# Optimization experiments

Measured on AMD Instinct MI355X. Metric: run time of the kernel, lower is better.

Reference implementation:

```python
import jax, jax.numpy as jnp
import numpy as np

HDIM = 128
SCALE = HDIM ** (-0.5)


def setup_inputs() -> dict:
    key = jax.random.key(0)
    ks = jax.random.split(key, 6)
    B, H, I, J, D = 4, 16, 2048, 2048, HDIM
    q = jax.random.normal(ks[0], (B, H, I, D), dtype=jnp.float32)
    kv = jax.random.normal(ks[1], (B, H, J, D), dtype=jnp.float32)
    # torch nn.Linear weights stored as [out_features, in_features]
    Wq = jax.random.normal(ks[2], (D, D), dtype=jnp.float32) * (D ** -0.5)
    Wkv = jax.random.normal(ks[3], (2 * D, D), dtype=jnp.float32) * (D ** -0.5)
    Wout = jax.random.normal(ks[4], (D, D), dtype=jnp.float32) * (D ** -0.5)
    bout = jax.random.normal(ks[5], (D,), dtype=jnp.float32) * 0.01
    return {"q": q, "kv": kv, "Wq": Wq, "Wkv": Wkv, "Wout": Wout, "bout": bout}


def reference(q, kv, Wq, Wkv, Wout, bout):
    # projections (torch Linear: x @ W.T)
    qp = jnp.einsum('bhid,ed->bhie', q, Wq)
    kvp = jnp.einsum('bhjd,ed->bhje', kv, Wkv)
    k, v = jnp.split(kvp, 2, axis=-1)
    # scaled dot-product cross attention, full score matrix [b,h,i,j]
    dots = jnp.einsum('bhid,bhjd->bhij', qp, k) * SCALE
    attn = jax.nn.softmax(dots, axis=-1)
    out = jnp.einsum('bhij,bhjd->bhid', attn, v)
    # output projection (dropout is identity at inference)
    return jnp.einsum('bhid,ed->bhie', out, Wout) + bout
```

## Files before the change

### kernel.cpp

```cpp
#include <hip/hip_runtime.h>
#include <hip/hip_bf16.h>
#include <math.h>

typedef __attribute__((ext_vector_type(8))) short bf16x8;
typedef __attribute__((ext_vector_type(4))) unsigned short u16x4;
typedef __attribute__((ext_vector_type(4))) float f32x4;

#define MFMA16(a, b, c) __builtin_amdgcn_mfma_f32_16x16x32_bf16(a, b, c, 0, 0, 0)

__device__ inline unsigned short f2bf(float x) {
  union { float f; unsigned u; } v; v.f = x;
  unsigned r = v.u + 0x7FFFu + ((v.u >> 16) & 1u);
  return (unsigned short)(r >> 16);
}

__device__ inline float exp2a(float x) {
  float r;
  asm("v_exp_f32 %0, %1" : "=v"(r) : "v"(x));
  return r;
}

__device__ inline void dma16(const unsigned short* g, unsigned short* l) {
  __builtin_amdgcn_global_load_lds(
      (const __attribute__((address_space(1))) unsigned int*)g,
      (__attribute__((address_space(3))) unsigned int*)l, 16, 0, 0);
}

__device__ unsigned short g_wbf[49152];

__global__ __launch_bounds__(256) void conv_w(
    const float* __restrict__ Wq, const float* __restrict__ Wkv)
{
  int idx = (blockIdx.x * 256 + threadIdx.x) * 4;
  const float* src; int off;
  if (idx < 16384) { src = Wq;  off = idx; }
  else             { src = Wkv; off = idx - 16384; }
  float4 v = *(const float4*)(src + off);
  u16x4 pk;
  pk.x = f2bf(v.x); pk.y = f2bf(v.y); pk.z = f2bf(v.z); pk.w = f2bf(v.w);
  *(u16x4*)&g_wbf[idx] = pk;
}

__global__ __launch_bounds__(256) void proj_q(
    const float* __restrict__ A, unsigned short* __restrict__ out0, float scale)
{
  const int mbase = blockIdx.x * 64;
  const unsigned short* Wb = g_wbf;

  __shared__ unsigned short a_s[64 * 136];
  __shared__ unsigned short w_s[128 * 136];

  const int tid = threadIdx.x;
  for (int p = 0; p < 8; ++p) {
    int r = p * 8 + (tid >> 5);
    int c = tid & 31;
    float4 v = ((const float4*)(A + (size_t)(mbase + r) * 128))[c];
    u16x4 pk;
    pk.x = f2bf(v.x); pk.y = f2bf(v.y); pk.z = f2bf(v.z); pk.w = f2bf(v.w);
    *(u16x4*)&a_s[r * 136 + c * 4] = pk;
  }
  {
    int r0 = tid >> 4, c = (tid & 15) * 8;
    for (int p = 0; p < 8; ++p) {
      int r = p * 16 + r0;
      *(bf16x8*)&w_s[r * 136 + c] = *(const bf16x8*)(Wb + (size_t)r * 128 + c);
    }
  }
  __syncthreads();

  const int wave = tid >> 6, lane = tid & 63, quad = lane >> 4, lr = lane & 15;
  f32x4 zero = {0.f, 0.f, 0.f, 0.f};
  f32x4 acc[8];
  for (int nb = 0; nb < 8; ++nb) acc[nb] = zero;
  for (int ks = 0; ks < 4; ++ks) {
    bf16x8 af = *(const bf16x8*)&a_s[(wave * 16 + lr) * 136 + ks * 32 + quad * 8];
    for (int nb = 0; nb < 8; ++nb) {
      bf16x8 bf = *(const bf16x8*)&w_s[(nb * 16 + lr) * 136 + ks * 32 + quad * 8];
      acc[nb] = MFMA16(af, bf, acc[nb]);
    }
  }
  for (int nb = 0; nb < 8; ++nb)
    for (int r = 0; r < 4; ++r) {
      int row = mbase + wave * 16 + quad * 4 + r;
      int col = nb * 16 + lr;
      out0[(size_t)row * 128 + col] = f2bf(acc[nb][r] * scale);
    }
}

__global__ __launch_bounds__(256) void proj_kv(
    const float* __restrict__ A,
    unsigned short* __restrict__ outK, unsigned short* __restrict__ outVT)
{
  const int mbase = blockIdx.x * 64;
  __shared__ unsigned short a_s[64 * 136];
  __shared__ unsigned short w_s[128 * 136];
  const int tid = threadIdx.x;

  for (int p = 0; p < 8; ++p) {
    int r = p * 8 + (tid >> 5);
    int c = tid & 31;
    float4 v = ((const float4*)(A + (size_t)(mbase + r) * 128))[c];
    u16x4 pk;
    pk.x = f2bf(v.x); pk.y = f2bf(v.y); pk.z = f2bf(v.z); pk.w = f2bf(v.w);
    *(u16x4*)&a_s[r * 136 + c * 4] = pk;
  }

  const int wave = tid >> 6, lane = tid & 63, quad = lane >> 4, lr = lane & 15;
  f32x4 zero = {0.f, 0.f, 0.f, 0.f};

  for (int nt = 0; nt < 2; ++nt) {
    __syncthreads();
    {
      const unsigned short* Wb = g_wbf + 16384 + nt * 16384;
      int r0 = tid >> 4, c = (tid & 15) * 8;
      for (int p = 0; p < 8; ++p) {
        int r = p * 16 + r0;
        *(bf16x8*)&w_s[r * 136 + c] = *(const bf16x8*)(Wb + (size_t)r * 128 + c);
      }
    }
    __syncthreads();

    f32x4 acc[8];
    for (int nb = 0; nb < 8; ++nb) acc[nb] = zero;
    for (int ks = 0; ks < 4; ++ks) {
      bf16x8 af = *(const bf16x8*)&a_s[(wave * 16 + lr) * 136 + ks * 32 + quad * 8];
      for (int nb = 0; nb < 8; ++nb) {
        bf16x8 bf = *(const bf16x8*)&w_s[(nb * 16 + lr) * 136 + ks * 32 + quad * 8];
        acc[nb] = MFMA16(af, bf, acc[nb]);
      }
    }

    if (nt == 0) {
      for (int nb = 0; nb < 8; ++nb)
        for (int r = 0; r < 4; ++r) {
          int row = mbase + wave * 16 + quad * 4 + r;
          int col = nb * 16 + lr;
          outK[(size_t)row * 128 + col] = f2bf(acc[nb][r]);
        }
    } else {
      int gm = mbase + wave * 16 + quad * 4;
      int bh = gm >> 11;
      int j  = gm & 2047;
      unsigned short* vt = outVT + (size_t)bh * 128 * 2048;
      for (int nb = 0; nb < 8; ++nb) {
        int col = nb * 16 + lr;
        u16x4 pk;
        pk.x = f2bf(acc[nb][0]); pk.y = f2bf(acc[nb][1]);
        pk.z = f2bf(acc[nb][2]); pk.w = f2bf(acc[nb][3]);
        *(u16x4*)&vt[(size_t)col * 2048 + j] = pk;
      }
    }
  }
}

__global__ __launch_bounds__(512, 2) void attn_fused(
    const unsigned short* __restrict__ qp,
    const unsigned short* __restrict__ kb,
    const unsigned short* __restrict__ vTb,
    const float* __restrict__ Wout,
    const float* __restrict__ bias,
    float* __restrict__ out)
{
  const int xcd = blockIdx.x & 7;
  const int loc = blockIdx.x >> 3;
  const int qt  = loc & 7;
  const int bh  = (loc >> 3) * 8 + xcd;
  const unsigned short* Q  = qp  + (size_t)bh * 2048 * 128 + (size_t)qt * 256 * 128;
  const unsigned short* K  = kb  + (size_t)bh * 2048 * 128;
  const unsigned short* VT = vTb + (size_t)bh * 128 * 2048;
  float* OUT = out + (size_t)bh * 2048 * 128 + (size_t)qt * 256 * 128;

  __shared__ unsigned short k_s [2][64 * 128];
  __shared__ unsigned short vT_s[2][128 * 64];
  __shared__ unsigned short p_s [256 * 64];
  __shared__ float redu_s[8][2][16];
  __shared__ unsigned short wout_s[128 * 136];

  const int tid = threadIdx.x;
  const int wave = tid >> 6, lane = tid & 63, quad = lane >> 4, lr = lane & 15;

  const int kw_i = wave * 2;
  const int rk0  = 4 * kw_i + (lane >> 4);
  const int rk1  = 4 * (kw_i + 1) + (lane >> 4);
  const int kgo0 = rk0 * 128 + ((lane & 15) ^ (rk0 & 15)) * 8;
  const int kgo1 = rk1 * 128 + ((lane & 15) ^ (rk1 & 15)) * 8;
  const int rv0  = 8 * kw_i + (lane >> 3);
  const int rv1  = 8 * (kw_i + 1) + (lane >> 3);
  const int vsc  = ((lane & 7) ^ ((lane >> 3) & 7)) * 8;
  const int vgo0 = rv0 * 2048 + vsc;
  const int vgo1 = rv1 * 2048 + vsc;
  const int klds0 = kw_i * 512, klds1 = kw_i * 512 + 512;

#define ISSUE_K(T, BUF) do { \
    const unsigned short* _kt = K + (size_t)(T) * 8192; \
    dma16(_kt + kgo0, &k_s[BUF][klds0]); \
    dma16(_kt + kgo1, &k_s[BUF][klds1]); } while (0)
#define ISSUE_V(T, BUF) do { \
    const unsigned short* _vt = VT + (size_t)(T) * 64; \
    dma16(_vt + vgo0, &vT_s[BUF][klds0]); \
    dma16(_vt + vgo1, &vT_s[BUF][klds1]); } while (0)

  bf16x8 qf[2][4];
#pragma unroll
  for (int mb = 0; mb < 2; ++mb)
#pragma unroll
    for (int ks = 0; ks < 4; ++ks)
      qf[mb][ks] = *(const bf16x8*)(Q + (size_t)(wave * 32 + mb * 16 + lr) * 128 + ks * 32 + quad * 8);
  __builtin_amdgcn_sched_barrier(0);
  ISSUE_K(0, 0);
  ISSUE_V(0, 0);
  ISSUE_K(1, 1);
  __builtin_amdgcn_sched_barrier(0);

  f32x4 zero = {0.f, 0.f, 0.f, 0.f};
  f32x4 o_acc[2][8];
  float m_i[2], l_i[2];
#pragma unroll
  for (int mb = 0; mb < 2; ++mb) {
#pragma unroll
    for (int db = 0; db < 8; ++db) o_acc[mb][db] = zero;
    m_i[mb] = -1e30f; l_i[mb] = 0.f;
  }
  int rescM = 0;

  asm volatile("s_waitcnt vmcnt(2)" ::: "memory");
  __builtin_amdgcn_s_barrier();
  __builtin_amdgcn_sched_barrier(0);
  ISSUE_V(1, 1);

#define STEP(JT, BUF) do { \
    f32x4 sT[2][4]; \
    _Pragma("unroll") \
    for (int mi = 0; mi < 2; ++mi) \
      _Pragma("unroll") \
      for (int jb = 0; jb < 4; ++jb) sT[mi][jb] = zero; \
    __builtin_amdgcn_s_setprio(1); \
    _Pragma("unroll") \
    for (int ks = 0; ks < 4; ++ks) { \
      _Pragma("unroll") \
      for (int jb = 0; jb < 4; ++jb) { \
        bf16x8 kfj = *(const bf16x8*)&k_s[BUF][(jb * 16 + lr) * 128 + (((ks * 4 + quad) ^ lr) << 3)]; \
        sT[0][jb] = MFMA16(kfj, qf[0][ks], sT[0][jb]); \
        sT[1][jb] = MFMA16(kfj, qf[1][ks], sT[1][jb]); \
      } \
    } \
    __builtin_amdgcn_s_setprio(0); \
    _Pragma("unroll") \
    for (int mi = 0; mi < 2; ++mi) { \
      const int mb = mi; \
      float mx = fmaxf(fmaxf(sT[mi][0][0], sT[mi][0][1]), fmaxf(sT[mi][0][2], sT[mi][0][3])); \
      _Pragma("unroll") \
      for (int jb = 1; jb < 4; ++jb) \
        mx = fmaxf(mx, fmaxf(fmaxf(sT[mi][jb][0], sT[mi][jb][1]), \
                             fmaxf(sT[mi][jb][2], sT[mi][jb][3]))); \
      mx = fmaxf(mx, __shfl_xor(mx, 16)); \
      mx = fmaxf(mx, __shfl_xor(mx, 32)); \
      if (!__all(mx - m_i[mb] <= 8.f)) {            \
        float mnew = fmaxf(m_i[mb], mx); \
        float alpha = exp2a(m_i[mb] - mnew); \
        m_i[mb] = mnew; \
        l_i[mb] *= alpha; \
        if (lane < 16) redu_s[wave][mb][lane] = alpha; \
        rescM |= (1 << (mb)); \
      } \
      float rs = 0.f; \
      const int prow = wave * 32 + mb * 16 + lr; \
      _Pragma("unroll") \
      for (int jb = 0; jb < 4; ++jb) { \
        float p0 = exp2a(sT[mi][jb][0] - m_i[mb]); \
        float p1 = exp2a(sT[mi][jb][1] - m_i[mb]); \
        float p2 = exp2a(sT[mi][jb][2] - m_i[mb]); \
        float p3 = exp2a(sT[mi][jb][3] - m_i[mb]); \
        rs += (p0 + p1) + (p2 + p3); \
        u16x4 pk; \
        pk.x = f2bf(p0); pk.y = f2bf(p1); pk.z = f2bf(p2); pk.w = f2bf(p3); \
        int c = jb * 2 + (quad >> 1); \
        *(u16x4*)&p_s[prow * 64 + ((c ^ (lr & 7)) << 3) + ((quad & 1) << 2)] = pk; \
      } \
      rs += __shfl_xor(rs, 16); \
      rs += __shfl_xor(rs, 32); \
      l_i[mb] += rs; \
    } \
    __builtin_amdgcn_s_barrier();         \
    __builtin_amdgcn_sched_barrier(0); \
    if ((JT) <= 29) ISSUE_K((JT) + 2, BUF); \
    _Pragma("unroll") \
    for (int mb = 0; mb < 2; ++mb) \
      if (rescM & (1 << (mb))) {                       \
        f32x4 av = *(const f32x4*)&redu_s[wave][mb][quad * 4]; \
        _Pragma("unroll") \
        for (int db = 0; db < 8; ++db) o_acc[mb][db] *= av; \
      } \
    rescM = 0; \
    __builtin_amdgcn_s_setprio(1); \
    _Pragma("unroll") \
    for (int ks2 = 0; ks2 < 2; ++ks2) { \
      const int pc = ((ks2 * 4 + quad) ^ (lr & 7)) << 3; \
      bf16x8 pf[2]; \
      _Pragma("unroll") \
      for (int mb = 0; mb < 2; ++mb) \
        pf[mb] = *(const bf16x8*)&p_s[(wave * 32 + mb * 16 + lr) * 64 + pc]; \
      _Pragma("unroll") \
      for (int db = 0; db < 8; ++db) { \
        bf16x8 vf = *(const bf16x8*)&vT_s[BUF][(db * 16 + lr) * 64 + pc]; \
        _Pragma("unroll") \
        for (int mb = 0; mb < 2; ++mb) \
          o_acc[mb][db] = MFMA16(pf[mb], vf, o_acc[mb][db]); \
      } \
    } \
    __builtin_amdgcn_s_setprio(0); \
    if ((JT) >= 30) { asm volatile("s_waitcnt vmcnt(0)" ::: "memory"); } \
    else            { asm volatile("s_waitcnt vmcnt(2)" ::: "memory"); } \
    __builtin_amdgcn_s_barrier();         \
    __builtin_amdgcn_sched_barrier(0); \
    if ((JT) <= 29) ISSUE_V((JT) + 2, BUF); \
  } while (0)

#pragma unroll 1
  for (int jtb = 0; jtb < 16; ++jtb) {
    const int jt0 = jtb * 2;
    STEP(jt0, 0);
    STEP(jt0 + 1, 1);
  }
#undef STEP
#undef ISSUE_K
#undef ISSUE_V

#pragma unroll
  for (int p = 0; p < 4; ++p) {
    int r = p * 32 + (tid >> 4);
    int c = (tid & 15) * 8;
    float4 v0 = *(const float4*)(Wout + (size_t)r * 128 + c);
    float4 v1 = *(const float4*)(Wout + (size_t)r * 128 + c + 4);
    u16x4 pk0, pk1;
    pk0.x = f2bf(v0.x); pk0.y = f2bf(v0.y); pk0.z = f2bf(v0.z); pk0.w = f2bf(v0.w);
    pk1.x = f2bf(v1.x); pk1.y = f2bf(v1.y); pk1.z = f2bf(v1.z); pk1.w = f2bf(v1.w);
    *(u16x4*)&wout_s[r * 136 + c] = pk0;
    *(u16x4*)&wout_s[r * 136 + c + 4] = pk1;
  }

#pragma unroll
  for (int mb = 0; mb < 2; ++mb)
    if (lane < 16) redu_s[wave][mb][lane] = l_i[mb];
#pragma unroll
  for (int mb = 0; mb < 2; ++mb) {
    f32x4 l4 = *(const f32x4*)&redu_s[wave][mb][quad * 4];
    f32x4 invv;
#pragma unroll
    for (int r = 0; r < 4; ++r) invv[r] = 1.f / l4[r];
#pragma unroll
    for (int db = 0; db < 8; ++db) o_acc[mb][db] *= invv;
  }

  __syncthreads();

  f32x4 acc2[2][8];
#pragma unroll
  for (int mb = 0; mb < 2; ++mb)
#pragma unroll
    for (int nb = 0; nb < 8; ++nb) acc2[mb][nb] = zero;

#pragma unroll
  for (int h = 0; h < 2; ++h) {
#pragma unroll
    for (int mb = 0; mb < 2; ++mb)
#pragma unroll
      for (int db2 = 0; db2 < 4; ++db2) {
        f32x4 o = o_acc[mb][h * 4 + db2];
#pragma unroll
        for (int r = 0; r < 4; ++r) {
          int row = mb * 16 + quad * 4 + r;
          int colh = db2 * 16 + lr;
          int chunk = colh >> 3, off = colh & 7;
          p_s[(wave * 32 + row) * 64 + ((chunk ^ (row & 7)) << 3) + off] = f2bf(o[r]);
        }
      }
#pragma unroll
    for (int ks = 0; ks < 2; ++ks) {
#pragma unroll
      for (int mb = 0; mb < 2; ++mb) {
        int arow = mb * 16 + lr;
        int kk = ks * 32 + quad * 8;
        int chunk = kk >> 3;
        bf16x8 af = *(const bf16x8*)&p_s[(wave * 32 + arow) * 64 + ((chunk ^ (arow & 7)) << 3)];
#pragma unroll
        for (int nb = 0; nb < 8; ++nb) {
          bf16x8 bf = *(const bf16x8*)&wout_s[(nb * 16 + lr) * 136 + h * 64 + kk];
          acc2[mb][nb] = MFMA16(af, bf, acc2[mb][nb]);
        }
      }
    }
  }

#pragma unroll
  for (int mb = 0; mb < 2; ++mb)
#pragma unroll
    for (int nb = 0; nb < 8; ++nb) {
      int col = nb * 16 + lr;
      float b = bias[col];
#pragma unroll
      for (int r = 0; r < 4; ++r) {
        int row = wave * 32 + mb * 16 + quad * 4 + r;
        OUT[(size_t)row * 128 + col] = acc2[mb][nb][r] + b;
      }
    }
}

extern "C" void kernel_launch(void* const* d_in, const int* in_sizes, int n_in,
                              void* d_out, int out_size, void* d_ws, size_t ws_size,
                              hipStream_t stream) {
  const float* q    = (const float*)d_in[0];
  const float* kv   = (const float*)d_in[1];
  const float* Wq   = (const float*)d_in[2];
  const float* Wkv  = (const float*)d_in[3];
  const float* Wout = (const float*)d_in[4];
  const float* bout = (const float*)d_in[5];
  float* out = (float*)d_out;

  const size_t NELEM = (size_t)131072 * 128;
  unsigned short* qp_b = (unsigned short*)d_ws;
  unsigned short* k_b  = qp_b + NELEM;
  unsigned short* vT_b = k_b + NELEM;

  const float SCALE2 = 0.08838834764831845f * 1.4426950408889634f;

  conv_w<<<dim3(48), 256, 0, stream>>>(Wq, Wkv);
  proj_q<<<dim3(2048), 256, 0, stream>>>(q, qp_b, SCALE2);
  proj_kv<<<dim3(2048), 256, 0, stream>>>(kv, k_b, vT_b);
  attn_fused<<<dim3(512), 512, 0, stream>>>(qp_b, k_b, vT_b, Wout, bout, out);
}
```

Baseline: 372.9 us.

## Merge Q and KV projection kernels and stage V-transpose through LDS

Combines the separate Q and KV projection launches into one grid of 4096 blocks, branching on block index, so both projections can run concurrently and one launch is dropped. The V-transpose output is now staged through shared memory and written as 16-byte contiguous row segments instead of scattered 8-byte writes with a 4KB stride. This adds extra barriers and LDS traffic in the KV branch.

```diff
diff --git a/kernel.cpp b/kernel.cpp
--- a/kernel.cpp
+++ b/kernel.cpp
@@ -41,77 +41,30 @@
   *(u16x4*)&g_wbf[idx] = pk;
 }
 
-__global__ __launch_bounds__(256) void proj_q(
-    const float* __restrict__ A, unsigned short* __restrict__ out0, float scale)
+__global__ __launch_bounds__(256) void proj_qkv(
+    const float* __restrict__ Aq, const float* __restrict__ Akv,
+    unsigned short* __restrict__ outQ, unsigned short* __restrict__ outK,
+    unsigned short* __restrict__ outVT, float scale)
 {
-  const int mbase = blockIdx.x * 64;
-  const unsigned short* Wb = g_wbf;
-
   __shared__ unsigned short a_s[64 * 136];
   __shared__ unsigned short w_s[128 * 136];
 
   const int tid = threadIdx.x;
-  for (int p = 0; p < 8; ++p) {
-    int r = p * 8 + (tid >> 5);
-    int c = tid & 31;
-    float4 v = ((const float4*)(A + (size_t)(mbase + r) * 128))[c];
-    u16x4 pk;
-    pk.x = f2bf(v.x); pk.y = f2bf(v.y); pk.z = f2bf(v.z); pk.w = f2bf(v.w);
-    *(u16x4*)&a_s[r * 136 + c * 4] = pk;
-  }
-  {
-    int r0 = tid >> 4, c = (tid & 15) * 8;
-    for (int p = 0; p < 8; ++p) {
-      int r = p * 16 + r0;
-      *(bf16x8*)&w_s[r * 136 + c] = *(const bf16x8*)(Wb + (size_t)r * 128 + c);
-    }
-  }
-  __syncthreads();
-
   const int wave = tid >> 6, lane = tid & 63, quad = lane >> 4, lr = lane & 15;
   f32x4 zero = {0.f, 0.f, 0.f, 0.f};
-  f32x4 acc[8];
-  for (int nb = 0; nb < 8; ++nb) acc[nb] = zero;
-  for (int ks = 0; ks < 4; ++ks) {
-    bf16x8 af = *(const bf16x8*)&a_s[(wave * 16 + lr) * 136 + ks * 32 + quad * 8];
-    for (int nb = 0; nb < 8; ++nb) {
-      bf16x8 bf = *(const bf16x8*)&w_s[(nb * 16 + lr) * 136 + ks * 32 + quad * 8];
-      acc[nb] = MFMA16(af, bf, acc[nb]);
-    }
-  }
-  for (int nb = 0; nb < 8; ++nb)
-    for (int r = 0; r < 4; ++r) {
-      int row = mbase + wave * 16 + quad * 4 + r;
-      int col = nb * 16 + lr;
-      out0[(size_t)row * 128 + col] = f2bf(acc[nb][r] * scale);
-    }
-}
-
-__global__ __launch_bounds__(256) void proj_kv(
-    const float* __restrict__ A,
-    unsigned short* __restrict__ outK, unsigned short* __restrict__ outVT)
-{
-  const int mbase = blockIdx.x * 64;
-  __shared__ unsigned short a_s[64 * 136];
-  __shared__ unsigned short w_s[128 * 136];
-  const int tid = threadIdx.x;
-
-  for (int p = 0; p < 8; ++p) {
-    int r = p * 8 + (tid >> 5);
-    int c = tid & 31;
-    float4 v = ((const float4*)(A + (size_t)(mbase + r) * 128))[c];
-    u16x4 pk;
-    pk.x = f2bf(v.x); pk.y = f2bf(v.y); pk.z = f2bf(v.z); pk.w = f2bf(v.w);
-    *(u16x4*)&a_s[r * 136 + c * 4] = pk;
-  }
-
-  const int wave = tid >> 6, lane = tid & 63, quad = lane >> 4, lr = lane & 15;
-  f32x4 zero = {0.f, 0.f, 0.f, 0.f};
-
-  for (int nt = 0; nt < 2; ++nt) {
-    __syncthreads();
+
+  if (blockIdx.x < 2048) {
+    const int mbase = blockIdx.x * 64;
+    for (int p = 0; p < 8; ++p) {
+      int r = p * 8 + (tid >> 5);
+      int c = tid & 31;
+      float4 v = ((const float4*)(Aq + (size_t)(mbase + r) * 128))[c];
+      u16x4 pk;
+      pk.x = f2bf(v.x); pk.y = f2bf(v.y); pk.z = f2bf(v.z); pk.w = f2bf(v.w);
+      *(u16x4*)&a_s[r * 136 + c * 4] = pk;
+    }
     {
-      const unsigned short* Wb = g_wbf + 16384 + nt * 16384;
+      const unsigned short* Wb = g_wbf;
       int r0 = tid >> 4, c = (tid & 15) * 8;
       for (int p = 0; p < 8; ++p) {
         int r = p * 16 + r0;
@@ -129,25 +82,69 @@
         acc[nb] = MFMA16(af, bf, acc[nb]);
       }
     }
-
-    if (nt == 0) {
-      for (int nb = 0; nb < 8; ++nb)
-        for (int r = 0; r < 4; ++r) {
-          int row = mbase + wave * 16 + quad * 4 + r;
-          int col = nb * 16 + lr;
-          outK[(size_t)row * 128 + col] = f2bf(acc[nb][r]);
+    for (int nb = 0; nb < 8; ++nb)
+      for (int r = 0; r < 4; ++r) {
+        int row = mbase + wave * 16 + quad * 4 + r;
+        int col = nb * 16 + lr;
+        outQ[(size_t)row * 128 + col] = f2bf(acc[nb][r] * scale);
+      }
+  } else {
+    const int mbase = (blockIdx.x - 2048) * 64;
+    for (int p = 0; p < 8; ++p) {
+      int r = p * 8 + (tid >> 5);
+      int c = tid & 31;
+      float4 v = ((const float4*)(Akv + (size_t)(mbase + r) * 128))[c];
+      u16x4 pk;
+      pk.x = f2bf(v.x); pk.y = f2bf(v.y); pk.z = f2bf(v.z); pk.w = f2bf(v.w);
+      *(u16x4*)&a_s[r * 136 + c * 4] = pk;
+    }
+
+    for (int nt = 0; nt < 2; ++nt) {
+      __syncthreads();
+      {
+        const unsigned short* Wb = g_wbf + 16384 + nt * 16384;
+        int r0 = tid >> 4, c = (tid & 15) * 8;
+        for (int p = 0; p < 8; ++p) {
+          int r = p * 16 + r0;
+          *(bf16x8*)&w_s[r * 136 + c] = *(const bf16x8*)(Wb + (size_t)r * 128 + c);
         }
-    } else {
-      int gm = mbase + wave * 16 + quad * 4;
-      int bh = gm >> 11;
-      int j  = gm & 2047;
-      unsigned short* vt = outVT + (size_t)bh * 128 * 2048;
-      for (int nb = 0; nb < 8; ++nb) {
-        int col = nb * 16 + lr;
-        u16x4 pk;
-        pk.x = f2bf(acc[nb][0]); pk.y = f2bf(acc[nb][1]);
-        pk.z = f2bf(acc[nb][2]); pk.w = f2bf(acc[nb][3]);
-        *(u16x4*)&vt[(size_t)col * 2048 + j] = pk;
+      }
+      __syncthreads();
+
+      f32x4 acc[8];
+      for (int nb = 0; nb < 8; ++nb) acc[nb] = zero;
+      for (int ks = 0; ks < 4; ++ks) {
+        bf16x8 af = *(const bf16x8*)&a_s[(wave * 16 + lr) * 136 + ks * 32 + quad * 8];
+        for (int nb = 0; nb < 8; ++nb) {
+          bf16x8 bf = *(const bf16x8*)&w_s[(nb * 16 + lr) * 136 + ks * 32 + quad * 8];
+          acc[nb] = MFMA16(af, bf, acc[nb]);
+        }
+      }
+
+      if (nt == 0) {
+        for (int nb = 0; nb < 8; ++nb)
+          for (int r = 0; r < 4; ++r) {
+            int row = mbase + wave * 16 + quad * 4 + r;
+            int col = nb * 16 + lr;
+            outK[(size_t)row * 128 + col] = f2bf(acc[nb][r]);
+          }
+      } else {
+        unsigned short* t_s = w_s;
+        __syncthreads();
+        const int jloc = wave * 16 + quad * 4;
+        for (int nb = 0; nb < 8; ++nb) {
+          u16x4 pk;
+          pk.x = f2bf(acc[nb][0]); pk.y = f2bf(acc[nb][1]);
+          pk.z = f2bf(acc[nb][2]); pk.w = f2bf(acc[nb][3]);
+          *(u16x4*)&t_s[(nb * 16 + lr) * 72 + jloc] = pk;
+        }
+        __syncthreads();
+        const int col = tid >> 1, hf = (tid & 1) * 32;
+        unsigned short* vt = outVT + (size_t)(mbase >> 11) * 128 * 2048
+                             + (size_t)col * 2048 + (mbase & 2047) + hf;
+        const unsigned short* ts = &t_s[col * 72 + hf];
+        for (int k2 = 0; k2 < 4; ++k2)
+          *(bf16x8*)(vt + k2 * 8) = *(const bf16x8*)(ts + k2 * 8);
       }
     }
   }
@@ -425,7 +422,6 @@
   const float SCALE2 = 0.08838834764831845f * 1.4426950408889634f;
 
   conv_w<<<dim3(48), 256, 0, stream>>>(Wq, Wkv);
-  proj_q<<<dim3(2048), 256, 0, stream>>>(q, qp_b, SCALE2);
-  proj_kv<<<dim3(2048), 256, 0, stream>>>(kv, k_b, vT_b);
+  proj_qkv<<<dim3(4096), 256, 0, stream>>>(q, kv, qp_b, k_b, vT_b, SCALE2);
   attn_fused<<<dim3(512), 512, 0, stream>>>(qp_b, k_b, vT_b, Wout, bout, out);
 }
```

Result: faster. 362.6 us (-2.8%).
